# Kernel tuning notes

Measured on AMD Instinct MI355X. Metric: run time of the kernel, lower is better.

## Reference

```python
import jax, jax.numpy as jnp
import numpy as np

N_VERTS = 200000
N_TETS = 800000
FREQ_NUM = 4
SCALE = 1.0
HID = 256
D_IN = 3 + 6 * FREQ_NUM  # 27

_TRI_TABLE = np.array([
    [-1,-1,-1,-1,-1,-1],[1,0,2,-1,-1,-1],[4,0,3,-1,-1,-1],[1,4,2,1,3,4],
    [3,1,5,-1,-1,-1],[2,3,0,2,5,3],[1,4,0,1,5,4],[4,2,5,-1,-1,-1],
    [4,5,2,-1,-1,-1],[4,1,0,4,5,1],[3,2,0,3,5,2],[1,3,5,-1,-1,-1],
    [4,1,2,4,3,1],[3,0,4,-1,-1,-1],[2,0,1,-1,-1,-1],[-1,-1,-1,-1,-1,-1]], dtype=np.int32)
_NUM_TRI = np.array([0,1,1,2,1,2,2,1,1,2,2,1,2,1,1,0], dtype=np.int32)
_BASE_EDGES = np.array([0,1,0,2,0,3,1,2,1,3,2,3], dtype=np.int32)


def _pos_enc(x):
    feats = [x]
    for i in range(FREQ_NUM):
        f = float(2 ** i) * np.pi / SCALE
        feats.append(jnp.sin(f * x))
        feats.append(jnp.cos(f * x))
    return jnp.concatenate(feats, axis=-1)  # [N, 27]


def _mlp_sdf(pos, w0, b0, w1, b1, w2, b2, w3, b3, wf, bf):
    h = jax.nn.relu(_pos_enc(pos) @ w0 + b0)
    for w, b in ((w1, b1), (w2, b2), (w3, b3)):
        h = jax.nn.relu(h @ w + b)
    return (h @ wf + bf)[:, 0]  # [N]


def setup_inputs() -> dict:
    key = jax.random.key(0)
    ks = jax.random.split(key, 12)
    def lin(k, fan_in, shape):
        return jax.random.normal(k, shape, jnp.float32) * (2.0 / fan_in) ** 0.5
    return {
        "pos": jax.random.normal(ks[0], (N_VERTS, 3), jnp.float32),
        "tet_fx4": jax.random.randint(ks[1], (N_TETS, 4), 0, N_VERTS, dtype=jnp.int32),
        "w0": lin(ks[2], D_IN, (D_IN, HID)), "b0": jnp.zeros((HID,), jnp.float32),
        "w1": lin(ks[3], HID, (HID, HID)), "b1": jnp.zeros((HID,), jnp.float32),
        "w2": lin(ks[4], HID, (HID, HID)), "b2": jnp.zeros((HID,), jnp.float32),
        "w3": lin(ks[5], HID, (HID, HID)), "b3": jnp.zeros((HID,), jnp.float32),
        "wf": lin(ks[6], HID, (HID, 1)), "bf": jnp.zeros((1,), jnp.float32),
    }


def reference(pos, tet_fx4, w0, b0, w1, b1, w2, b2, w3, b3, wf, bf):
    # SDF from the positional-encoding MLP (DMTetGeometry)
    sdf = _mlp_sdf(pos, w0, b0, w1, b1, w2, b2, w3, b3, wf, bf)

    # --- marching tetrahedra (DMTet.__call__) ---
    occ = sdf > 0                       # [N]
    occ_fx4 = occ[tet_fx4]              # [F,4]
    occ_sum = occ_fx4.sum(-1)
    valid = (occ_sum > 0) & (occ_sum < 4)
    vt = tet_fx4[valid]                 # [V,4] tets crossed by the surface
    occ_v = occ_fx4[valid]              # [V,4]

    # all 6 edges per valid tet, sorted so (lo, hi)
    e = vt[:, _BASE_EDGES].reshape(-1, 2)                         # [6V,2]
    e = jnp.stack([jnp.minimum(e[:, 0], e[:, 1]),
                   jnp.maximum(e[:, 0], e[:, 1])], axis=1)
    uniq, inv = jnp.unique(e, axis=0, return_inverse=True)        # dedup edges
    inv = inv.reshape(-1)

    # edges whose endpoints straddle the zero level set
    cross = occ[uniq].sum(-1) == 1                                 # [U]
    mapping = jnp.where(cross, jnp.cumsum(cross) - 1, -1)          # compact ids
    idx_map = mapping[inv].reshape(-1, 6)                          # [V,6]
    interp_v = uniq[cross]                                         # [M,2]

    # linear interpolation of crossing vertices along each crossing edge
    p = pos[interp_v]                                              # [M,2,3]
    s = sdf[interp_v]                                              # [M,2]
    denom = s[:, 0] - s[:, 1]                                      # s0 + (-s1)
    verts = (p[:, 0] * (-s[:, 1])[:, None] + p[:, 1] * s[:, 0][:, None]) / denom[:, None]

    # triangle table lookup
    tetindex = (occ_v.astype(jnp.int32) * (2 ** jnp.arange(4, dtype=jnp.int32))).sum(-1)
    ntri = jnp.asarray(_NUM_TRI)[tetindex]
    tri = jnp.asarray(_TRI_TABLE)[tetindex]
    m1 = ntri == 1
    m2 = ntri == 2
    f1 = jnp.take_along_axis(idx_map[m1], tri[m1][:, :3], axis=1).reshape(-1, 3)
    f2 = jnp.take_along_axis(idx_map[m2], tri[m2][:, :6], axis=1).reshape(-1, 3)
    faces = jnp.concatenate([f1, f2], axis=0)
    return verts, faces
```

## Files before the change

kernel.cpp:

```cpp
#include <hip/hip_runtime.h>
#include <cstdint>
#include <cstddef>

#define NV 200000
#define NT 800000
#define ROWS 64
#define MBLK 3125
#define NBLK 3125
#define NSEGS 196
#define PCAP 4096

typedef unsigned int u32;
typedef unsigned long long u64;

typedef __attribute__((ext_vector_type(8))) _Float16 half8;
typedef __attribute__((ext_vector_type(4))) float f32x4;
#define MFMA16F __builtin_amdgcn_mfma_f32_16x16x32_f16

__constant__ int c_tri[16][6] = {
  {-1,-1,-1,-1,-1,-1},{1,0,2,-1,-1,-1},{4,0,3,-1,-1,-1},{1,4,2,1,3,4},
  {3,1,5,-1,-1,-1},{2,3,0,2,5,3},{1,4,0,1,5,4},{4,2,5,-1,-1,-1},
  {4,5,2,-1,-1,-1},{4,1,0,4,5,1},{3,2,0,3,5,2},{1,3,5,-1,-1,-1},
  {4,1,2,4,3,1},{3,0,4,-1,-1,-1},{2,0,1,-1,-1,-1},{-1,-1,-1,-1,-1,-1}};
__constant__ int c_ntri[16] = {0,1,1,2,1,2,2,1,1,2,2,1,2,1,1,0};
__constant__ int c_be[12] = {0,1,0,2,0,3,1,2,1,3,2,3};

__device__ __forceinline__ void split2(float x, _Float16& h, _Float16& m){
  h = (_Float16)x;
  const float r = x - (float)h;
  m = (_Float16)(r * 2048.0f);
}

__global__ void split_weights(const float* __restrict__ w0, const float* __restrict__ w1,
                              const float* __restrict__ w2, const float* __restrict__ w3,
                              _Float16* __restrict__ wp, u32* __restrict__ segcur)
{
  const int t = blockIdx.x*256 + threadIdx.x;
  if (t < 256) segcur[t] = 0u;
  int base, psz, c, kg, n, kvalid;
  const float* w;
  if (t < 1024){
    base = 0; psz = 8192; c = 0;
    kg = t >> 8; n = t & 255;
    w = w0; kvalid = 27;
  } else {
    int r = t - 1024;
    const int l = r >> 13;
    r &= 8191;
    c = r >> 10; kg = (r >> 8) & 3; n = r & 255;
    base = 16384 + l*131072; psz = 65536;
    w = (l==0) ? w1 : (l==1) ? w2 : w3;
    kvalid = 256;
  }
  half8 hv, mv;
#pragma unroll
  for (int j=0;j<8;j++){
    const int k = c*32 + kg*8 + j;
    const float val = (k < kvalid) ? w[k*256 + n] : 0.f;
    _Float16 h, m; split2(val, h, m);
    hv[j] = h; mv[j] = m;
  }
  const int off = (c*256 + n)*32 + kg*8;
  *(half8*)(wp + base + off) = hv;
  *(half8*)(wp + base + psz + off) = mv;
}

template<int NC, bool LAST>
__device__ __forceinline__ void layer_run(
    const _Float16* __restrict__ Wl, const float* __restrict__ Bv,
    const float* __restrict__ wfv,
    _Float16 (*Af)[ROWS][264], float (*part)[8],
    int lane, int wv)
{
  const int l15 = lane & 15, q = lane >> 4;
  const int col0 = wv * 32;
  f32x4 g0[4][2], g1[4][2];
#pragma unroll
  for (int i=0;i<4;i++)
#pragma unroll
    for (int j=0;j<2;j++){ g0[i][j] = (f32x4){0.f,0.f,0.f,0.f}; g1[i][j] = (f32x4){0.f,0.f,0.f,0.f}; }

  const _Float16* bp = Wl + (u32)((col0 + l15)*32 + q*8);
  half8 bA[2][2], bB[2][2];

  auto loadB = [&](int c, half8 (*dst)[2]){
#pragma unroll
    for (int p=0;p<2;p++)
#pragma unroll
      for (int nt=0;nt<2;nt++)
        dst[p][nt] = *(const half8*)(bp + (p*NC + c)*8192 + nt*512);
  };
  auto compute = [&](int c, const half8 (*bb)[2]){
#pragma unroll
    for (int mt=0;mt<4;mt++){
      const _Float16* ap = &Af[0][mt*16 + l15][c*32 + q*8];
      const half8 ah = *(const half8*)(ap);
      const half8 am = *(const half8*)(ap + ROWS*264);
#pragma unroll
      for (int nt=0;nt<2;nt++){
        g0[mt][nt] = MFMA16F(ah, bb[0][nt], g0[mt][nt], 0,0,0);
        g1[mt][nt] = MFMA16F(ah, bb[1][nt], g1[mt][nt], 0,0,0);
        g1[mt][nt] = MFMA16F(am, bb[0][nt], g1[mt][nt], 0,0,0);
      }
    }
  };

  loadB(0, bA);
  if (NC == 1){
    compute(0, bA);
  } else {
#pragma unroll 1
    for (int ch=0; ch<NC/2; ch++){
      const int c0 = 2*ch;
      loadB(c0+1, bB);
      compute(c0, bA);
      if (c0+2 < NC) loadB(c0+2, bA);
      compute(c0+1, bB);
    }
  }
  __syncthreads();

  const float S = 4.8828125e-4f;
  if (!LAST){
#pragma unroll
    for (int nt=0;nt<2;nt++){
      const int col = col0 + nt*16 + l15;
      const float bias = Bv[col];
#pragma unroll
      for (int mt=0;mt<4;mt++)
#pragma unroll
        for (int reg=0;reg<4;reg++){
          const int row = mt*16 + q*4 + reg;
          const float v = fmaxf(g0[mt][nt][reg] + S*g1[mt][nt][reg] + bias, 0.f);
          _Float16 h,m; split2(v,h,m);
          Af[0][row][col] = h; Af[1][row][col] = m;
        }
    }
  } else {
    float pr[4][4];
#pragma unroll
    for (int mt=0;mt<4;mt++)
#pragma unroll
      for (int reg=0;reg<4;reg++) pr[mt][reg] = 0.f;
#pragma unroll
    for (int nt=0;nt<2;nt++){
      const int col = col0 + nt*16 + l15;
      const float bias = Bv[col];
      const float w = wfv[col];
#pragma unroll
      for (int mt=0;mt<4;mt++)
#pragma unroll
        for (int reg=0;reg<4;reg++)
          pr[mt][reg] += fmaxf(g0[mt][nt][reg] + S*g1[mt][nt][reg] + bias, 0.f) * w;
    }
#pragma unroll
    for (int s=1;s<16;s<<=1)
#pragma unroll
      for (int mt=0;mt<4;mt++)
#pragma unroll
        for (int reg=0;reg<4;reg++)
          pr[mt][reg] += __shfl_xor(pr[mt][reg], s, 64);
    if (l15 == 0){
#pragma unroll
      for (int mt=0;mt<4;mt++)
#pragma unroll
        for (int reg=0;reg<4;reg++)
          part[mt*16 + q*4 + reg][wv] = pr[mt][reg];
    }
  }
  __syncthreads();
}

__global__ __launch_bounds__(512,4) void mlp_mfma(
    const float* __restrict__ pos, const _Float16* __restrict__ wp,
    const float* __restrict__ b0, const float* __restrict__ b1,
    const float* __restrict__ b2, const float* __restrict__ b3,
    const float* __restrict__ wf, const float* __restrict__ bf,
    float* __restrict__ sdf)
{
  __shared__ _Float16 Af[2][ROWS][264];
  __shared__ float part[ROWS][8];
  const int tid = threadIdx.x;
  const int lane = tid & 63, wv = tid >> 6;
  const int row0 = blockIdx.x * ROWS;

  if ((blockIdx.x & 256) && (blockIdx.x < 512)){
#pragma unroll 1
    for (int i=0;i<13;i++) __builtin_amdgcn_s_sleep(15);
  }

#pragma unroll
  for (int it=0; it<4; it++){
    const int idx = it*512 + tid;
    const int r = idx & 63, f = idx >> 6;
    float val = 0.f;
    if (f < 3){
      val = pos[(row0 + r)*3 + f];
    } else if (f < 27){
      const int g = (f-3)/6, rem = (f-3)%6;
      const int d = rem % 3;
      const float x = pos[(row0 + r)*3 + d];
      const float fr = (float)(1 << g) * 3.14159265358979323846f;
      val = (rem < 3) ? sinf(fr*x) : cosf(fr*x);
    }
    _Float16 h,m; split2(val,h,m);
    Af[0][r][f] = h; Af[1][r][f] = m;
  }
  __syncthreads();

  layer_run<1,false>(wp + 0,      b0, nullptr, Af, part, lane, wv);
  layer_run<8,false>(wp + 16384,  b1, nullptr, Af, part, lane, wv);
  layer_run<8,false>(wp + 147456, b2, nullptr, Af, part, lane, wv);
  layer_run<8,true >(wp + 278528, b3, wf,      Af, part, lane, wv);

  if (tid < ROWS){
    float s = 0.f;
#pragma unroll
    for (int w=0; w<8; w++) s += part[tid][w];
    sdf[row0 + tid] = s + bf[0];
  }
}

__device__ __forceinline__ u32 wave_scan_incl(u32 v, int lane){
#pragma unroll
  for (int s=1;s<64;s<<=1){
    const u32 y = __shfl_up(v, s, 64);
    if (lane >= s) v += y;
  }
  return v;
}
__device__ __forceinline__ u32 block_scan_fast(u32 v, u32* sh4, int tid){
  const int lane = tid & 63, wv = tid >> 6;
  const u32 incl = wave_scan_incl(v, lane);
  if (lane == 63) sh4[wv] = incl;
  __syncthreads();
  u32 base = 0;
#pragma unroll
  for (int w=0;w<3;w++) if (w < wv) base += sh4[w];
  return incl + base;
}
__device__ __forceinline__ u64 bscan_u64(u64 v, u64* sh, int tid){
  sh[tid]=v; __syncthreads();
#pragma unroll
  for (int s=1;s<256;s<<=1){
    const u64 y = (tid>=s) ? sh[tid-s] : 0ull;
    __syncthreads();
    sh[tid] += y;
    __syncthreads();
  }
  return sh[tid];
}

__global__ void tet_pairs(const int* __restrict__ tet, const float* __restrict__ sdf,
    unsigned char* __restrict__ codes, u32* __restrict__ tscan, u32* __restrict__ tsum,
    u32* __restrict__ segcur, u64* __restrict__ pairs)
{
  __shared__ u32 sh4[4];
  const int tid = threadIdx.x;
  const int t = blockIdx.x*256 + tid;
  const int4 v = *(const int4*)(&tet[4*t]);
  const int o0 = sdf[v.x] > 0.f;
  const int o1 = sdf[v.y] > 0.f;
  const int o2 = sdf[v.z] > 0.f;
  const int o3 = sdf[v.w] > 0.f;
  const int code = o0 | (o1<<1) | (o2<<2) | (o3<<3);
  codes[t] = (unsigned char)code;
  const int nt = c_ntri[code];
  if (nt > 0){
    const int vv[4] = {v.x, v.y, v.z, v.w};
    const int oc[4] = {o0,o1,o2,o3};
#pragma unroll
    for (int e=0;e<6;e++){
      const int ia = c_be[2*e], ib = c_be[2*e+1];
      if (oc[ia] != oc[ib]){
        const int p = vv[ia], q = vv[ib];
        const int lo = p<q ? p : q, hi = p<q ? q : p;
        const int seg = lo >> 10;
        const u32 slot = atomicAdd(&segcur[seg], 1u);
        if (slot < PCAP)
          pairs[(size_t)seg*PCAP + slot] = ((u64)(u32)lo << 32) | (u32)hi;
      }
    }
  }
  const u32 my = (u32)(nt==1) | ((u32)(nt==2)<<16);
  const u32 incl = block_scan_fast(my, sh4, tid);
  tscan[t] = incl - my;
  if (tid == 255) tsum[blockIdx.x] = incl;
}

__global__ void seg_process(const u64* __restrict__ pairs_in, const u32* __restrict__ segcur,
    u64* __restrict__ uq, u32* __restrict__ ucnt, u32* __restrict__ ucnt_ex,
    u32* __restrict__ usum, const u32* __restrict__ tsum, u64* __restrict__ tsumE,
    u32* __restrict__ meta)
{
  const int tid = threadIdx.x;
  if (blockIdx.x == NSEGS){
    __shared__ u64 sh64[256];
    u64 loc[13]; u64 tot = 0ull;
#pragma unroll
    for (int i=0;i<13;i++){
      const int idx = tid*13 + i;
      const u32 p = (idx < NBLK) ? tsum[idx] : 0u;
      const u64 u = (u64)(p & 0xffffu) | ((u64)(p >> 16) << 32);
      loc[i] = u; tot += u;
    }
    const u64 incl = bscan_u64(tot, sh64, tid);
    u64 run = incl - tot;
#pragma unroll
    for (int i=0;i<13;i++){
      const int idx = tid*13 + i;
      if (idx < NBLK) tsumE[idx] = run;
      run += loc[i];
    }
    if (tid == 255){ meta[0] = (u32)(incl & 0xffffffffull); meta[1] = (u32)(incl >> 32); }
    return;
  }

  __shared__ u64 P[PCAP];
  __shared__ u32 sh4[4];
  __shared__ u32 shbase;
  const int seg = blockIdx.x;
  int n = (int)segcur[seg];
  if (n > PCAP) n = PCAP;
  int np = 1; while (np < n) np <<= 1;

  for (int i=tid; i<np; i+=256)
    P[i] = (i < n) ? pairs_in[(size_t)seg*PCAP + i] : ~0ull;
  if (tid == 0) shbase = 0u;
  __syncthreads();

  for (int k=2; k<=np; k<<=1){
    for (int j=k>>1; j>0; j>>=1){
      for (int i=tid; i<np; i+=256){
        const int ij = i ^ j;
        if (ij > i){
          const u64 a = P[i], b = P[ij];
          const bool up = ((i & k) == 0);
          if ((a > b) == up){ P[i] = b; P[ij] = a; }
        }
      }
      __syncthreads();
    }
  }

  for (int c=0; c<n; c+=256){
    const int i = c + tid;
    u64 key = 0ull; u32 f = 0u;
    if (i < n){
      key = P[i];
      f = (i == 0 || P[i] != P[i-1]) ? 1u : 0u;
    }
    __syncthreads();
    const u32 incl = block_scan_fast(f, sh4, tid);
    const u32 base = shbase;
    if (f) P[base + incl - 1u] = key;
    __syncthreads();
    if (tid == 255) shbase = base + incl;
    __syncthreads();
  }
  const int uc = (int)shbase;

  for (int i=tid; i<uc; i+=256) uq[(size_t)seg*PCAP + i] = P[i];

  const int lo0 = seg << 10;
  for (int c=0; c<1024; c+=256){
    const int lo = lo0 + c + tid;
    if (lo < NV){
      const u64 kl = (u64)(u32)lo << 32;
      const u64 kh = (u64)(u32)(lo+1) << 32;
      int a=0, b=uc;
      while (a < b){ const int m=(a+b)>>1; if (P[m] < kl) a=m+1; else b=m; }
      const int lb = a;
      b = uc;
      while (a < b){ const int m=(a+b)>>1; if (P[m] < kh) a=m+1; else b=m; }
      ucnt_ex[lo] = (u32)lb;
      ucnt[lo] = (u32)(a - lb);
    }
  }
  if (tid == 0) usum[seg] = (u32)uc;
}

__global__ void emit_all(const int* __restrict__ tet, const float* __restrict__ pos,
    const float* __restrict__ sdf, const unsigned char* __restrict__ codes,
    const u32* __restrict__ tscan, const u64* __restrict__ tsumE, const u32* __restrict__ meta,
    const u64* __restrict__ uq, const u32* __restrict__ ucnt, const u32* __restrict__ ucnt_ex,
    const u32* __restrict__ usum, float* __restrict__ out, int out_size)
{
  __shared__ u32 sh4[4];
  __shared__ u32 shu[NSEGS];
  __shared__ u32 shM;
  const int tid = threadIdx.x;
  {
    const u32 v = (tid < NSEGS) ? usum[tid] : 0u;
    const u32 incl = block_scan_fast(v, sh4, tid);
    if (tid < NSEGS) shu[tid] = incl - v;
    if (tid == NSEGS-1) shM = incl;
    __syncthreads();
  }

  if (blockIdx.x < NSEGS){
    const int seg = blockIdx.x;
    const int uc = (int)usum[seg];
    const u32 base = shu[seg];
    for (int i=tid; i<uc; i+=256){
      const u64 key = uq[(size_t)seg*PCAP + i];
      const int lo = (int)(key >> 32);
      const int hi = (int)(key & 0xffffffffull);
      const float s0 = sdf[lo], s1 = sdf[hi];
      const float d = s0 - s1;
      const float vx = (pos[3*lo  ]*(-s1) + pos[3*hi  ]*s0) / d;
      const float vy = (pos[3*lo+1]*(-s1) + pos[3*hi+1]*s0) / d;
      const float vz = (pos[3*lo+2]*(-s1) + pos[3*hi+2]*s0) / d;
      const long long w = 3ll*(long long)(base + (u32)i);
      if (w + 3 <= (long long)out_size){
        out[w] = vx; out[w+1] = vy; out[w+2] = vz;
      }
    }
  } else {
    const int t = (blockIdx.x - NSEGS)*256 + tid;
    const int code = codes[t];
    const int nt = c_ntri[code];
    if (nt == 0) return;
    const u64 tb = tsumE[t>>8];
    const u32 ts = tscan[t];
    const u32 n1e = (u32)(tb & 0xffffffffull) + (ts & 0xffffu);
    const u32 n2e = (u32)(tb >> 32) + (ts >> 16);
    const u32 N1 = meta[0];
    const u32 M  = shM;
    const u32 fb = (nt==1) ? n1e : (N1 + 2u*n2e);
    const int4 v = *(const int4*)(&tet[4*t]);
    const int vv[4] = {v.x, v.y, v.z, v.w};
    for (int r=0;r<nt;r++){
      for (int k=0;k<3;k++){
        const int e = c_tri[code][3*r+k];
        const int ia = c_be[2*e], ib = c_be[2*e+1];
        const int p = vv[ia], q = vv[ib];
        const int lo = p<q ? p : q, hi = p<q ? q : p;
        const int seg = lo >> 10;
        const u32 st = ucnt_ex[lo];
        const int u = (int)ucnt[lo];
        const u64* b = uq + (size_t)seg*PCAP + st;
        int id = -1;
        for (int j=0;j<u;j++){
          if ((int)(b[j] & 0xffffffffull) == hi){ id = (int)(shu[seg] + st) + j; break; }
        }
        const long long w = 3ll*(long long)M + 3ll*(long long)(fb + (u32)r) + k;
        if (w < (long long)out_size && id >= 0) out[w] = (float)id;
      }
    }
  }
}

extern "C" void kernel_launch(void* const* d_in, const int* in_sizes, int n_in,
                              void* d_out, int out_size, void* d_ws, size_t ws_size,
                              hipStream_t stream)
{
  (void)in_sizes; (void)n_in; (void)ws_size;
  const float* pos = (const float*)d_in[0];
  const int*   tet = (const int*)d_in[1];
  const float* w0 = (const float*)d_in[2];
  const float* b0 = (const float*)d_in[3];
  const float* w1 = (const float*)d_in[4];
  const float* b1 = (const float*)d_in[5];
  const float* w2 = (const float*)d_in[6];
  const float* b2 = (const float*)d_in[7];
  const float* w3 = (const float*)d_in[8];
  const float* b3 = (const float*)d_in[9];
  const float* wf = (const float*)d_in[10];
  const float* bf = (const float*)d_in[11];
  float* out = (float*)d_out;
  char* ws = (char*)d_ws;

  float*         sdf   = (float*)(ws + 0);
  unsigned char* codes = (unsigned char*)(ws + 800000);
  u32* tscan   = (u32*)(ws + 1600000);
  u32* tsum    = (u32*)(ws + 4800000);
  u64* tsumE   = (u64*)(ws + 4812800);
  u32* segcur  = (u32*)(ws + 4837888);
  u32* usum    = (u32*)(ws + 4838912);
  u32* meta    = (u32*)(ws + 4839936);
  u32* ucnt    = (u32*)(ws + 4840000);
  u32* ucnt_ex = (u32*)(ws + 5640000);
  _Float16* wp = (_Float16*)(ws + 6440000);
  u64* pairs   = (u64*)(ws + 7259200);

  split_weights<<<100,256,0,stream>>>(w0,w1,w2,w3,wp,segcur);
  mlp_mfma<<<MBLK,512,0,stream>>>(pos,wp,b0,b1,b2,b3,wf,bf,sdf);

  tet_pairs<<<NBLK,256,0,stream>>>(tet,sdf,codes,tscan,tsum,segcur,pairs);
  seg_process<<<NSEGS+1,256,0,stream>>>(pairs,segcur,pairs,ucnt,ucnt_ex,usum,tsum,tsumE,meta);
  emit_all<<<NSEGS+NBLK,256,0,stream>>>(tet,pos,sdf,codes,tscan,tsumE,meta,
                                        pairs,ucnt,ucnt_ex,usum,out,out_size);
}
```

Baseline: 466.5 us.

## Switch MLP from 16x16x32 to 32x32x16 MFMA with 2x4 wave tiling

```diff
diff --git a/kernel.cpp b/kernel.cpp
--- a/kernel.cpp
+++ b/kernel.cpp
@@ -9,13 +9,16 @@
 #define NBLK 3125
 #define NSEGS 196
 #define PCAP 4096
+#define AST 264
+#define PST (ROWS*AST)
 
 typedef unsigned int u32;
 typedef unsigned long long u64;
 
 typedef __attribute__((ext_vector_type(8))) _Float16 half8;
 typedef __attribute__((ext_vector_type(4))) float f32x4;
-#define MFMA16F __builtin_amdgcn_mfma_f32_16x16x32_f16
+typedef __attribute__((ext_vector_type(16))) float f32x16;
+#define MFMA32F __builtin_amdgcn_mfma_f32_32x32x16_f16
 
 __constant__ int c_tri[16][6] = {
   {-1,-1,-1,-1,-1,-1},{1,0,2,-1,-1,-1},{4,0,3,-1,-1,-1},{1,4,2,1,3,4},
@@ -40,14 +43,14 @@
   int base, psz, c, kg, n, kvalid;
   const float* w;
   if (t < 1024){
-    base = 0; psz = 8192; c = 0;
-    kg = t >> 8; n = t & 255;
+    base = 0; psz = 8192;
+    c = t >> 9; kg = (t >> 8) & 1; n = t & 255;
     w = w0; kvalid = 27;
   } else {
     int r = t - 1024;
     const int l = r >> 13;
     r &= 8191;
-    c = r >> 10; kg = (r >> 8) & 3; n = r & 255;
+    c = r >> 9; kg = (r >> 8) & 1; n = r & 255;
     base = 16384 + l*131072; psz = 65536;
     w = (l==0) ? w1 : (l==1) ? w2 : w3;
     kvalid = 256;
@@ -55,32 +58,34 @@
   half8 hv, mv;
 #pragma unroll
   for (int j=0;j<8;j++){
-    const int k = c*32 + kg*8 + j;
+    const int k = c*16 + kg*8 + j;
     const float val = (k < kvalid) ? w[k*256 + n] : 0.f;
     _Float16 h, m; split2(val, h, m);
     hv[j] = h; mv[j] = m;
   }
-  const int off = (c*256 + n)*32 + kg*8;
+  const int off = (c*256 + n)*16 + kg*8;
   *(half8*)(wp + base + off) = hv;
   *(half8*)(wp + base + psz + off) = mv;
 }
 
-template<int NC, bool LAST>
+template<int NCH, int PSZ, bool LAST>
 __device__ __forceinline__ void layer_run(
     const _Float16* __restrict__ Wl, const float* __restrict__ Bv,
     const float* __restrict__ wfv,
-    _Float16 (*Af)[ROWS][264], float (*part)[8],
+    _Float16 (*Af)[ROWS][AST], float (*part)[5],
     int lane, int wv)
 {
-  const int l15 = lane & 15, q = lane >> 4;
-  const int col0 = wv * 32;
-  f32x4 g0[4][2], g1[4][2];
-#pragma unroll
-  for (int i=0;i<4;i++)
-#pragma unroll
-    for (int j=0;j<2;j++){ g0[i][j] = (f32x4){0.f,0.f,0.f,0.f}; g1[i][j] = (f32x4){0.f,0.f,0.f,0.f}; }
-
-  const _Float16* bp = Wl + (u32)((col0 + l15)*32 + q*8);
+  const int l31 = lane & 31, hi = lane >> 5;
+  const int rt = wv >> 2, cg = wv & 3;
+  const int col0 = cg * 64;
+  f32x16 g0[2], g1[2];
+#pragma unroll
+  for (int nt=0; nt<2; nt++){
+#pragma unroll
+    for (int r=0; r<16; r++){ g0[nt][r] = 0.f; g1[nt][r] = 0.f; }
+  }
+
+  const _Float16* bp = Wl + (u32)((col0 + l31)*16 + hi*8);
   half8 bA[2][2], bB[2][2];
 
   auto loadB = [&](int c, half8 (*dst)[2]){
@@ -88,35 +93,28 @@
     for (int p=0;p<2;p++)
 #pragma unroll
       for (int nt=0;nt<2;nt++)
-        dst[p][nt] = *(const half8*)(bp + (p*NC + c)*8192 + nt*512);
+        dst[p][nt] = *(const half8*)(bp + p*PSZ + c*4096 + nt*512);
   };
   auto compute = [&](int c, const half8 (*bb)[2]){
-#pragma unroll
-    for (int mt=0;mt<4;mt++){
-      const _Float16* ap = &Af[0][mt*16 + l15][c*32 + q*8];
-      const half8 ah = *(const half8*)(ap);
-      const half8 am = *(const half8*)(ap + ROWS*264);
-#pragma unroll
-      for (int nt=0;nt<2;nt++){
-        g0[mt][nt] = MFMA16F(ah, bb[0][nt], g0[mt][nt], 0,0,0);
-        g1[mt][nt] = MFMA16F(ah, bb[1][nt], g1[mt][nt], 0,0,0);
-        g1[mt][nt] = MFMA16F(am, bb[0][nt], g1[mt][nt], 0,0,0);
-      }
+    const _Float16* ap = &Af[0][rt*32 + l31][c*16 + hi*8];
+    const half8 ah = *(const half8*)(ap);
+    const half8 am = *(const half8*)(ap + PST);
+#pragma unroll
+    for (int nt=0;nt<2;nt++){
+      g0[nt] = MFMA32F(ah, bb[0][nt], g0[nt], 0,0,0);
+      g1[nt] = MFMA32F(ah, bb[1][nt], g1[nt], 0,0,0);
+      g1[nt] = MFMA32F(am, bb[0][nt], g1[nt], 0,0,0);
     }
   };
 
   loadB(0, bA);
-  if (NC == 1){
-    compute(0, bA);
-  } else {
 #pragma unroll 1
-    for (int ch=0; ch<NC/2; ch++){
-      const int c0 = 2*ch;
-      loadB(c0+1, bB);
-      compute(c0, bA);
-      if (c0+2 < NC) loadB(c0+2, bA);
-      compute(c0+1, bB);
-    }
+  for (int ch=0; ch<NCH/2; ch++){
+    const int c0 = 2*ch;
+    loadB(c0+1, bB);
+    compute(c0, bA);
+    if (c0+2 < NCH) loadB(c0+2, bA);
+    compute(c0+1, bB);
   }
   __syncthreads();
 
@@ -124,48 +122,38 @@
   if (!LAST){
 #pragma unroll
     for (int nt=0;nt<2;nt++){
-      const int col = col0 + nt*16 + l15;
+      const int col = col0 + nt*32 + l31;
       const float bias = Bv[col];
 #pragma unroll
-      for (int mt=0;mt<4;mt++)
-#pragma unroll
-        for (int reg=0;reg<4;reg++){
-          const int row = mt*16 + q*4 + reg;
-          const float v = fmaxf(g0[mt][nt][reg] + S*g1[mt][nt][reg] + bias, 0.f);
-          _Float16 h,m; split2(v,h,m);
-          Af[0][row][col] = h; Af[1][row][col] = m;
-        }
+      for (int reg=0;reg<16;reg++){
+        const int row = rt*32 + (reg&3) + 8*(reg>>2) + 4*hi;
+        const float v = fmaxf(g0[nt][reg] + S*g1[nt][reg] + bias, 0.f);
+        _Float16 h,m; split2(v,h,m);
+        Af[0][row][col] = h; Af[1][row][col] = m;
+      }
     }
   } else {
-    float pr[4][4];
-#pragma unroll
-    for (int mt=0;mt<4;mt++)
-#pragma unroll
-      for (int reg=0;reg<4;reg++) pr[mt][reg] = 0.f;
+    float pr[16];
+#pragma unroll
+    for (int reg=0;reg<16;reg++) pr[reg] = 0.f;
 #pragma unroll
     for (int nt=0;nt<2;nt++){
-      const int col = col0 + nt*16 + l15;
+      const int col = col0 + nt*32 + l31;
       const float bias = Bv[col];
       const float w = wfv[col];
 #pragma unroll
-      for (int mt=0;mt<4;mt++)
-#pragma unroll
-        for (int reg=0;reg<4;reg++)
-          pr[mt][reg] += fmaxf(g0[mt][nt][reg] + S*g1[mt][nt][reg] + bias, 0.f) * w;
-    }
-#pragma unroll
-    for (int s=1;s<16;s<<=1)
-#pragma unroll
-      for (int mt=0;mt<4;mt++)
-#pragma unroll
-        for (int reg=0;reg<4;reg++)
-          pr[mt][reg] += __shfl_xor(pr[mt][reg], s, 64);
-    if (l15 == 0){
-#pragma unroll
-      for (int mt=0;mt<4;mt++)
-#pragma unroll
-        for (int reg=0;reg<4;reg++)
-          part[mt*16 + q*4 + reg][wv] = pr[mt][reg];
+      for (int reg=0;reg<16;reg++)
+        pr[reg] += fmaxf(g0[nt][reg] + S*g1[nt][reg] + bias, 0.f) * w;
+    }
+#pragma unroll
+    for (int s=1;s<32;s<<=1)
+#pragma unroll
+      for (int reg=0;reg<16;reg++)
+        pr[reg] += __shfl_xor(pr[reg], s, 64);
+    if (l31 == 0){
+#pragma unroll
+      for (int reg=0;reg<16;reg++)
+        part[rt*32 + (reg&3) + 8*(reg>>2) + 4*hi][cg] = pr[reg];
     }
   }
   __syncthreads();
@@ -178,16 +166,11 @@
     const float* __restrict__ wf, const float* __restrict__ bf,
     float* __restrict__ sdf)
 {
-  __shared__ _Float16 Af[2][ROWS][264];
-  __shared__ float part[ROWS][8];
+  __shared__ _Float16 Af[2][ROWS][AST];
+  __shared__ float part[ROWS][5];
   const int tid = threadIdx.x;
   const int lane = tid & 63, wv = tid >> 6;
   const int row0 = blockIdx.x * ROWS;
-
-  if ((blockIdx.x & 256) && (blockIdx.x < 512)){
-#pragma unroll 1
-    for (int i=0;i<13;i++) __builtin_amdgcn_s_sleep(15);
-  }
 
 #pragma unroll
   for (int it=0; it<4; it++){
@@ -208,15 +191,13 @@
   }
   __syncthreads();
 
-  layer_run<1,false>(wp + 0,      b0, nullptr, Af, part, lane, wv);
-  layer_run<8,false>(wp + 16384,  b1, nullptr, Af, part, lane, wv);
-  layer_run<8,false>(wp + 147456, b2, nullptr, Af, part, lane, wv);
-  layer_run<8,true >(wp + 278528, b3, wf,      Af, part, lane, wv);
+  layer_run< 2,  8192,false>(wp + 0,      b0, nullptr, Af, part, lane, wv);
+  layer_run<16, 65536,false>(wp + 16384,  b1, nullptr, Af, part, lane, wv);
+  layer_run<16, 65536,false>(wp + 147456, b2, nullptr, Af, part, lane, wv);
+  layer_run<16, 65536,true >(wp + 278528, b3, wf,      Af, part, lane, wv);
 
   if (tid < ROWS){
-    float s = 0.f;
-#pragma unroll
-    for (int w=0; w<8; w++) s += part[tid][w];
+    float s = part[tid][0] + part[tid][1] + part[tid][2] + part[tid][3];
     sdf[row0 + tid] = s + bf[0];
   }
 }
```

After: 497.5 us. 1.07x slower.

## Double MLP block tile to 128 rows with 2x4 wave grid per block

Applied to the files above, without the earlier changes.

```diff
diff --git a/kernel.cpp b/kernel.cpp
--- a/kernel.cpp
+++ b/kernel.cpp
@@ -4,11 +4,13 @@
 
 #define NV 200000
 #define NT 800000
-#define ROWS 64
-#define MBLK 3125
+#define ROWS 128
+#define MBLK 1563
 #define NBLK 3125
 #define NSEGS 196
 #define PCAP 4096
+#define AST 264
+#define PST (ROWS*AST)
 
 typedef unsigned int u32;
 typedef unsigned long long u64;
@@ -65,39 +67,41 @@
   *(half8*)(wp + base + psz + off) = mv;
 }
 
-template<int NC, bool LAST>
+template<int NC, int PSZ, bool LAST>
 __device__ __forceinline__ void layer_run(
     const _Float16* __restrict__ Wl, const float* __restrict__ Bv,
     const float* __restrict__ wfv,
-    _Float16 (*Af)[ROWS][264], float (*part)[8],
+    _Float16 (*Af)[ROWS][AST], float (*part)[5],
     int lane, int wv)
 {
   const int l15 = lane & 15, q = lane >> 4;
-  const int col0 = wv * 32;
-  f32x4 g0[4][2], g1[4][2];
+  const int rh = wv & 1, cs = wv >> 1;
+  const int row_base = rh * 64;
+  const int col0 = cs * 64;
+  f32x4 g0[4][4], g1[4][4];
 #pragma unroll
   for (int i=0;i<4;i++)
 #pragma unroll
-    for (int j=0;j<2;j++){ g0[i][j] = (f32x4){0.f,0.f,0.f,0.f}; g1[i][j] = (f32x4){0.f,0.f,0.f,0.f}; }
+    for (int j=0;j<4;j++){ g0[i][j] = (f32x4){0.f,0.f,0.f,0.f}; g1[i][j] = (f32x4){0.f,0.f,0.f,0.f}; }
 
   const _Float16* bp = Wl + (u32)((col0 + l15)*32 + q*8);
-  half8 bA[2][2], bB[2][2];
-
-  auto loadB = [&](int c, half8 (*dst)[2]){
+  half8 bA[2][4], bB[2][4];
+
+  auto loadB = [&](int c, half8 (*dst)[4]){
 #pragma unroll
     for (int p=0;p<2;p++)
 #pragma unroll
-      for (int nt=0;nt<2;nt++)
-        dst[p][nt] = *(const half8*)(bp + (p*NC + c)*8192 + nt*512);
+      for (int nt=0;nt<4;nt++)
+        dst[p][nt] = *(const half8*)(bp + p*PSZ + c*8192 + nt*512);
   };
-  auto compute = [&](int c, const half8 (*bb)[2]){
+  auto compute = [&](int c, const half8 (*bb)[4]){
 #pragma unroll
     for (int mt=0;mt<4;mt++){
-      const _Float16* ap = &Af[0][mt*16 + l15][c*32 + q*8];
+      const _Float16* ap = &Af[0][row_base + mt*16 + l15][c*32 + q*8];
       const half8 ah = *(const half8*)(ap);
-      const half8 am = *(const half8*)(ap + ROWS*264);
-#pragma unroll
-      for (int nt=0;nt<2;nt++){
+      const half8 am = *(const half8*)(ap + PST);
+#pragma unroll
+      for (int nt=0;nt<4;nt++){
         g0[mt][nt] = MFMA16F(ah, bb[0][nt], g0[mt][nt], 0,0,0);
         g1[mt][nt] = MFMA16F(ah, bb[1][nt], g1[mt][nt], 0,0,0);
         g1[mt][nt] = MFMA16F(am, bb[0][nt], g1[mt][nt], 0,0,0);
@@ -123,14 +127,14 @@
   const float S = 4.8828125e-4f;
   if (!LAST){
 #pragma unroll
-    for (int nt=0;nt<2;nt++){
+    for (int nt=0;nt<4;nt++){
       const int col = col0 + nt*16 + l15;
       const float bias = Bv[col];
 #pragma unroll
       for (int mt=0;mt<4;mt++)
 #pragma unroll
         for (int reg=0;reg<4;reg++){
-          const int row = mt*16 + q*4 + reg;
+          const int row = row_base + mt*16 + q*4 + reg;
           const float v = fmaxf(g0[mt][nt][reg] + S*g1[mt][nt][reg] + bias, 0.f);
           _Float16 h,m; split2(v,h,m);
           Af[0][row][col] = h; Af[1][row][col] = m;
@@ -143,7 +147,7 @@
 #pragma unroll
       for (int reg=0;reg<4;reg++) pr[mt][reg] = 0.f;
 #pragma unroll
-    for (int nt=0;nt<2;nt++){
+    for (int nt=0;nt<4;nt++){
       const int col = col0 + nt*16 + l15;
       const float bias = Bv[col];
       const float w = wfv[col];
@@ -165,58 +169,54 @@
       for (int mt=0;mt<4;mt++)
 #pragma unroll
         for (int reg=0;reg<4;reg++)
-          part[mt*16 + q*4 + reg][wv] = pr[mt][reg];
+          part[row_base + mt*16 + q*4 + reg][cs] = pr[mt][reg];
     }
   }
   __syncthreads();
 }
 
-__global__ __launch_bounds__(512,4) void mlp_mfma(
+__global__ __launch_bounds__(512,2) void mlp_mfma(
     const float* __restrict__ pos, const _Float16* __restrict__ wp,
     const float* __restrict__ b0, const float* __restrict__ b1,
     const float* __restrict__ b2, const float* __restrict__ b3,
     const float* __restrict__ wf, const float* __restrict__ bf,
     float* __restrict__ sdf)
 {
-  __shared__ _Float16 Af[2][ROWS][264];
-  __shared__ float part[ROWS][8];
+  __shared__ _Float16 Af[2][ROWS][AST];
+  __shared__ float part[ROWS][5];
   const int tid = threadIdx.x;
   const int lane = tid & 63, wv = tid >> 6;
   const int row0 = blockIdx.x * ROWS;
 
-  if ((blockIdx.x & 256) && (blockIdx.x < 512)){
-#pragma unroll 1
-    for (int i=0;i<13;i++) __builtin_amdgcn_s_sleep(15);
-  }
-
-#pragma unroll
-  for (int it=0; it<4; it++){
+#pragma unroll
+  for (int it=0; it<8; it++){
     const int idx = it*512 + tid;
-    const int r = idx & 63, f = idx >> 6;
+    const int r = idx & 127, f = idx >> 7;
+    const int gr = row0 + r;
     float val = 0.f;
-    if (f < 3){
-      val = pos[(row0 + r)*3 + f];
-    } else if (f < 27){
-      const int g = (f-3)/6, rem = (f-3)%6;
-      const int d = rem % 3;
-      const float x = pos[(row0 + r)*3 + d];
-      const float fr = (float)(1 << g) * 3.14159265358979323846f;
-      val = (rem < 3) ? sinf(fr*x) : cosf(fr*x);
+    if (gr < NV){
+      if (f < 3){
+        val = pos[gr*3 + f];
+      } else if (f < 27){
+        const int g = (f-3)/6, rem = (f-3)%6;
+        const int d = rem % 3;
+        const float x = pos[gr*3 + d];
+        const float fr = (float)(1 << g) * 3.14159265358979323846f;
+        val = (rem < 3) ? sinf(fr*x) : cosf(fr*x);
+      }
     }
     _Float16 h,m; split2(val,h,m);
     Af[0][r][f] = h; Af[1][r][f] = m;
   }
   __syncthreads();
 
-  layer_run<1,false>(wp + 0,      b0, nullptr, Af, part, lane, wv);
-  layer_run<8,false>(wp + 16384,  b1, nullptr, Af, part, lane, wv);
-  layer_run<8,false>(wp + 147456, b2, nullptr, Af, part, lane, wv);
-  layer_run<8,true >(wp + 278528, b3, wf,      Af, part, lane, wv);
-
-  if (tid < ROWS){
-    float s = 0.f;
-#pragma unroll
-    for (int w=0; w<8; w++) s += part[tid][w];
+  layer_run<1,  8192,false>(wp + 0,      b0, nullptr, Af, part, lane, wv);
+  layer_run<8, 65536,false>(wp + 16384,  b1, nullptr, Af, part, lane, wv);
+  layer_run<8, 65536,false>(wp + 147456, b2, nullptr, Af, part, lane, wv);
+  layer_run<8, 65536,true >(wp + 278528, b3, wf,      Af, part, lane, wv);
+
+  if (tid < ROWS && row0 + tid < NV){
+    float s = part[tid][0] + part[tid][1] + part[tid][2] + part[tid][3];
     sdf[row0 + tid] = s + bf[0];
   }
 }
```

Result: no change. 475.8 us (+2.0%).
